# Kernel tuning notes

Measured on AMD Instinct MI355X. Metric: run time of the kernel, lower is better.

## Reference

```python
import jax, jax.numpy as jnp
import numpy as np

N_EMBD = 1024
N_HEAD = 16
HEAD = N_EMBD // N_HEAD


def setup_inputs() -> dict:
    key = jax.random.key(0)
    ks = jax.random.split(key, 5)
    B, T = 2, 2048
    s = 1.0 / np.sqrt(N_EMBD)
    return {
        "x": jax.random.normal(ks[0], (B, T, N_EMBD), dtype=jnp.float32),
        "w_attn": jax.random.normal(ks[1], (N_EMBD, 3 * N_EMBD), dtype=jnp.float32) * s,
        "b_attn": jnp.zeros((3 * N_EMBD,), dtype=jnp.float32),
        "w_proj": jax.random.normal(ks[2], (N_EMBD, N_EMBD), dtype=jnp.float32) * s,
        "b_proj": jnp.zeros((N_EMBD,), dtype=jnp.float32),
    }


def reference(x, w_attn, b_attn, w_proj, b_proj):
    B, T, C = x.shape
    qkv = x @ w_attn + b_attn                      # [B,T,3C]
    q, k, v = jnp.split(qkv, 3, axis=-1)
    def heads(t):
        return t.reshape(B, T, N_HEAD, HEAD).transpose(0, 2, 1, 3)  # [B,H,T,D]
    q, k, v = heads(q), heads(k), heads(v)
    scale = 1.0 / np.sqrt(HEAD).astype(np.float32)
    scores = jnp.einsum('bhqd,bhkd->bhqk', q, k) * scale
    causal = jnp.tril(jnp.ones((T, T), dtype=bool))
    scores = jnp.where(causal, scores, -jnp.inf)
    attn = jax.nn.softmax(scores, axis=-1)
    out = jnp.einsum('bhqk,bhkd->bhqd', attn, v)   # [B,H,T,D]
    out = out.transpose(0, 2, 1, 3).reshape(B, T, C)
    return out @ w_proj + b_proj
```

## Files before the change

### kernel.cpp

```cpp
#include <hip/hip_runtime.h>
#include <stdint.h>

#define N_EMBD 1024
#define N_HEADv 16
#define HEADv 64
#define Bv 2
#define Tv 2048
#define BT (Bv*Tv)
#define C3 (3*N_EMBD)

typedef __attribute__((ext_vector_type(8))) short bf16x8;
typedef __attribute__((ext_vector_type(4))) float f32x4;

typedef __attribute__((address_space(3))) uint32_t lds_u32;
typedef const __attribute__((address_space(1))) uint32_t glb_u32;

__device__ __forceinline__ void gload_lds16(const void* g, void* l){
  __builtin_amdgcn_global_load_lds((glb_u32*)g, (lds_u32*)l, 16, 0, 0);
}

__device__ __forceinline__ unsigned short f2bf(float f){
  union { float f; uint32_t u; } v; v.f = f;
  uint32_t u = v.u;
  uint32_t r = u + 0x7FFFu + ((u>>16)&1u);
  return (unsigned short)(r>>16);
}
__device__ __forceinline__ uint32_t f2bf_fast(float f){
  union { float f; uint32_t u; } v; v.f = f;
  return (v.u + 0x8000u) >> 16;
}
__device__ __forceinline__ float bf2f(unsigned short s){
  union { uint32_t u; float f; } v; v.u = ((uint32_t)s)<<16; return v.f;
}

__global__ void k_cvt_bf16(const float* __restrict__ in, unsigned short* __restrict__ out, long n){
  long i = ((long)blockIdx.x*blockDim.x + threadIdx.x)*8;
  if(i >= n) return;
  float4 a = *reinterpret_cast<const float4*>(in+i);
  float4 b = *reinterpret_cast<const float4*>(in+i+4);
  union { int4 v; unsigned short s[8]; } o;
  o.s[0]=f2bf(a.x); o.s[1]=f2bf(a.y); o.s[2]=f2bf(a.z); o.s[3]=f2bf(a.w);
  o.s[4]=f2bf(b.x); o.s[5]=f2bf(b.y); o.s[6]=f2bf(b.z); o.s[7]=f2bf(b.w);
  *reinterpret_cast<int4*>(out+i) = o.v;
}

__global__ void k_transpose_bf16(const float* __restrict__ in, unsigned short* __restrict__ out, int K, int N){
  __shared__ float tile[64][65];
  int n0 = blockIdx.x*64, k0 = blockIdx.y*64;
  int t = threadIdx.x;
  #pragma unroll
  for(int p=0;p<4;p++){
    int row = (t>>4) + p*16;
    int col4 = (t&15)*4;
    float4 v = *reinterpret_cast<const float4*>(&in[(size_t)(k0+row)*N + n0 + col4]);
    tile[row][col4+0]=v.x; tile[row][col4+1]=v.y; tile[row][col4+2]=v.z; tile[row][col4+3]=v.w;
  }
  __syncthreads();
  #pragma unroll
  for(int p=0;p<4;p++){
    int nrow = (t>>4) + p*16;
    int kc = (t&15)*4;
    ushort4 o;
    o.x = f2bf(tile[kc+0][nrow]);
    o.y = f2bf(tile[kc+1][nrow]);
    o.z = f2bf(tile[kc+2][nrow]);
    o.w = f2bf(tile[kc+3][nrow]);
    *reinterpret_cast<ushort4*>(&out[(size_t)(n0+nrow)*K + k0 + kc]) = o;
  }
}

template<int MODE>
__global__ __launch_bounds__(256) void k_gemm(
    const unsigned short* __restrict__ A,
    const unsigned short* __restrict__ Bt,
    const float* __restrict__ bias,
    void* __restrict__ Cout,
    int M, int N, int K)
{
  const int BK=64;
  const int TSZ=128*BK;
  __shared__ unsigned short As[2*TSZ];
  __shared__ unsigned short Bs[2*TSZ];
  int m0 = blockIdx.y*128, n0 = blockIdx.x*128;
  int t = threadIdx.x, lane = t&63, wid = t>>6;
  int wm = (wid>>1)*64, wn = (wid&1)*64;
  int g = lane>>4, r16 = lane&15;
  int rl  = lane>>3;
  int cle = (((lane&7) ^ rl) * 8);
  int rsw = r16 & 7;
  f32x4 acc[4][4] = {};

  #pragma unroll
  for(int c=0;c<4;c++){
    int rb = wid*32 + c*8;
    gload_lds16(&A [(size_t)(m0+rb+rl)*K + cle], &As[rb*BK]);
    gload_lds16(&Bt[(size_t)(n0+rb+rl)*K + cle], &Bs[rb*BK]);
  }
  __syncthreads();

  const int NIT = K/BK;
  for(int it=0; it<NIT; ++it){
    int cur = it & 1;
    if(it+1 < NIT){
      int k0 = (it+1)*BK;
      int nxt = (cur^1)*TSZ;
      #pragma unroll
      for(int c=0;c<4;c++){
        int rb = wid*32 + c*8;
        gload_lds16(&A [(size_t)(m0+rb+rl)*K + k0 + cle], &As[nxt + rb*BK]);
        gload_lds16(&Bt[(size_t)(n0+rb+rl)*K + k0 + cle], &Bs[nxt + rb*BK]);
      }
    }
    const unsigned short* Ab = &As[cur*TSZ];
    const unsigned short* Bb = &Bs[cur*TSZ];
    bf16x8 af[2][4], bfr[2][4];
    #pragma unroll
    for(int ks=0;ks<2;ks++){
      #pragma unroll
      for(int mi=0;mi<4;mi++)
        af[ks][mi]  = *reinterpret_cast<const bf16x8*>(&Ab[(wm+mi*16+r16)*BK + (((ks*4+g)^rsw)*8)]);
      #pragma unroll
      for(int ni=0;ni<4;ni++)
        bfr[ks][ni] = *reinterpret_cast<const bf16x8*>(&Bb[(wn+ni*16+r16)*BK + (((ks*4+g)^rsw)*8)]);
    }
    __builtin_amdgcn_s_setprio(1);
    #pragma unroll
    for(int ks=0;ks<2;ks++)
      #pragma unroll
      for(int mi=0;mi<4;mi++)
        #pragma unroll
        for(int ni=0;ni<4;ni++){
          if(MODE==0)
            acc[mi][ni] = __builtin_amdgcn_mfma_f32_16x16x32_bf16(af[ks][mi], bfr[ks][ni], acc[mi][ni], 0,0,0);
          else
            acc[mi][ni] = __builtin_amdgcn_mfma_f32_16x16x32_bf16(bfr[ks][ni], af[ks][mi], acc[mi][ni], 0,0,0);
        }
    __builtin_amdgcn_s_setprio(0);
    __syncthreads();
  }

  if(MODE==0){
    int which = (n0+wn)>>10;
    int h = ((n0+wn)&1023)>>6;
    int bb = m0>>11;
    int tt0 = (m0&2047) + wm;
    unsigned short* base = (unsigned short*)Cout;
    if(which < 2){
      unsigned short* dst = base + (size_t)which*BT*N_EMBD
                          + (((size_t)bb*N_HEADv + h)*Tv + tt0)*HEADv;
      #pragma unroll
      for(int ni=0;ni<4;ni++){
        float bv = bias[n0+wn+ni*16+r16];
        int d = ni*16 + r16;
        #pragma unroll
        for(int mi=0;mi<4;mi++)
          #pragma unroll
          for(int reg=0;reg<4;reg++){
            int tt = mi*16 + g*4 + reg;
            dst[(size_t)tt*HEADv + d] = f2bf(acc[mi][ni][reg] + bv);
          }
      }
    } else {
      unsigned short* dst = base + 2ll*BT*N_EMBD
                          + (((size_t)bb*N_HEADv + h)*HEADv)*Tv + tt0;
      #pragma unroll
      for(int ni=0;ni<4;ni++){
        float bv = bias[n0+wn+ni*16+r16];
        int d = ni*16 + r16;
        #pragma unroll
        for(int mi=0;mi<4;mi++)
          #pragma unroll
          for(int reg=0;reg<4;reg++){
            int tt = mi*16 + g*4 + reg;
            dst[(size_t)d*Tv + tt] = f2bf(acc[mi][ni][reg] + bv);
          }
      }
    }
  } else {
    float* out = (float*)Cout;
    #pragma unroll
    for(int mi=0;mi<4;mi++){
      int m = m0+wm+mi*16+r16;
      #pragma unroll
      for(int ni=0;ni<4;ni++){
        int n = n0+wn+ni*16+g*4;
        float4 b4 = *reinterpret_cast<const float4*>(&bias[n]);
        float4 o4;
        o4.x = acc[mi][ni][0] + b4.x;
        o4.y = acc[mi][ni][1] + b4.y;
        o4.z = acc[mi][ni][2] + b4.z;
        o4.w = acc[mi][ni][3] + b4.w;
        *reinterpret_cast<float4*>(&out[(size_t)m*N + n]) = o4;
      }
    }
  }
}

__global__ __launch_bounds__(256) void k_attn(
    const unsigned short* __restrict__ QKV,
    unsigned short* __restrict__ O,
    unsigned short* __restrict__ partO,
    float2* __restrict__ stats)
{
  __shared__ unsigned short Ks[2][64][64];
  __shared__ unsigned short Vs[2][64][64];
  __shared__ unsigned short Ps[4][16][64];
  int blk = blockIdx.x;
  int bh = blk & 31;
  int j  = blk >> 5;
  int qt, kt0, ktN; bool single;
  if(j < 16)      { qt = 16+j;  kt0 = 0;  ktN = 16;    single = false; }
  else if(j < 32) { qt = 47-j;  kt0 = 16; ktN = qt+1;  single = false; }
  else            { qt = 47-j;  kt0 = 0;  ktN = qt+1;  single = true;  }

  int t = threadIdx.x, lane=t&63, wid=t>>6;
  int g = lane>>4, r16 = lane&15;
  const unsigned short* Qp  = QKV + (size_t)bh*Tv*HEADv;
  const unsigned short* Kp  = QKV + (size_t)BT*N_EMBD + (size_t)bh*Tv*HEADv;
  const unsigned short* Vtp = QKV + 2ll*BT*N_EMBD + (size_t)bh*HEADv*Tv;
  int q0 = qt*64 + wid*16;

  bf16x8 aq[2];
  #pragma unroll
  for(int kb=0;kb<2;kb++)
    aq[kb] = *reinterpret_cast<const bf16x8*>(&Qp[(size_t)(q0+r16)*HEADv + kb*32 + g*8]);

  f32x4 oacc[4] = {};
  float m2 = -1e30f, l = 0.f;

  int r0 = t>>3, c0 = (t&7)*8;
  int r1 = r0 + 32;
  int sw0 = c0 ^ ((r0&7)<<3);
  int sw1 = c0 ^ ((r1&7)<<3);
  int rsw = (r16&7)<<3;

  int4 kc0, kc1, vc0, vc1;
  kc0 = *reinterpret_cast<const int4*>(&Kp [(size_t)(kt0*64+r0)*HEADv + c0]);
  kc1 = *reinterpret_cast<const int4*>(&Kp [(size_t)(kt0*64+r1)*HEADv + c0]);
  vc0 = *reinterpret_cast<const int4*>(&Vtp[(size_t)r0*Tv + kt0*64 + c0]);
  vc1 = *reinterpret_cast<const int4*>(&Vtp[(size_t)r1*Tv + kt0*64 + c0]);
  *reinterpret_cast<int4*>(&Ks[0][r0][sw0]) = kc0;
  *reinterpret_cast<int4*>(&Ks[0][r1][sw1]) = kc1;
  *reinterpret_cast<int4*>(&Vs[0][r0][sw0]) = vc0;
  *reinterpret_cast<int4*>(&Vs[0][r1][sw1]) = vc1;
  if(ktN - kt0 > 1){
    kc0 = *reinterpret_cast<const int4*>(&Kp [(size_t)((kt0+1)*64+r0)*HEADv + c0]);
    kc1 = *reinterpret_cast<const int4*>(&Kp [(size_t)((kt0+1)*64+r1)*HEADv + c0]);
    vc0 = *reinterpret_cast<const int4*>(&Vtp[(size_t)r0*Tv + (kt0+1)*64 + c0]);
    vc1 = *reinterpret_cast<const int4*>(&Vtp[(size_t)r1*Tv + (kt0+1)*64 + c0]);
  }
  __syncthreads();

  for(int kt=kt0; kt<ktN; ++kt){
    int cur = kt & 1;
    if(kt+1 < ktN){
      *reinterpret_cast<int4*>(&Ks[cur^1][r0][sw0]) = kc0;
      *reinterpret_cast<int4*>(&Ks[cur^1][r1][sw1]) = kc1;
      *reinterpret_cast<int4*>(&Vs[cur^1][r0][sw0]) = vc0;
      *reinterpret_cast<int4*>(&Vs[cur^1][r1][sw1]) = vc1;
      if(kt+2 < ktN){
        kc0 = *reinterpret_cast<const int4*>(&Kp [(size_t)((kt+2)*64+r0)*HEADv + c0]);
        kc1 = *reinterpret_cast<const int4*>(&Kp [(size_t)((kt+2)*64+r1)*HEADv + c0]);
        vc0 = *reinterpret_cast<const int4*>(&Vtp[(size_t)r0*Tv + (kt+2)*64 + c0]);
        vc1 = *reinterpret_cast<const int4*>(&Vtp[(size_t)r1*Tv + (kt+2)*64 + c0]);
      }
    }

    f32x4 sacc[4];
    __builtin_amdgcn_s_setprio(1);
    #pragma unroll
    for(int nb=0;nb<4;nb++){
      sacc[nb] = (f32x4){0.f,0.f,0.f,0.f};
      #pragma unroll
      for(int kb=0;kb<2;kb++){
        bf16x8 bk = *reinterpret_cast<const bf16x8*>(&Ks[cur][nb*16+r16][(kb*32+g*8) ^ rsw]);
        sacc[nb] = __builtin_amdgcn_mfma_f32_16x16x32_bf16(bk, aq[kb], sacc[nb],0,0,0);
      }
    }
    __builtin_amdgcn_s_setprio(0);

    const float SC = 0.18033688f;
    bool diag = (kt == qt);
    float pv[4][4];
    float mxnb[4];
    #pragma unroll
    for(int nb=0;nb<4;nb++){
      #pragma unroll
      for(int reg=0;reg<4;reg++){
        float s = sacc[nb][reg] * SC;
        if(diag){
          int keyin = nb*16 + g*4 + reg;
          if(keyin > wid*16 + r16) s = -1e30f;
        }
        pv[nb][reg] = s;
      }
      mxnb[nb] = fmaxf(fmaxf(pv[nb][0],pv[nb][1]), fmaxf(pv[nb][2],pv[nb][3]));
    }
    float mx = fmaxf(fmaxf(mxnb[0],mxnb[1]), fmaxf(mxnb[2],mxnb[3]));
    mx = fmaxf(mx, __shfl_xor(mx, 16, 64));
    mx = fmaxf(mx, __shfl_xor(mx, 32, 64));

    if(!__all(mx - m2 <= 11.5f)){
      float mn = fmaxf(m2, mx);
      float alpha = __builtin_amdgcn_exp2f(m2 - mn);
      l *= alpha;
      #pragma unroll
      for(int nb=0;nb<4;nb++)
        #pragma unroll
        for(int reg=0;reg<4;reg++) oacc[nb][reg] *= alpha;
      m2 = mn;
    }

    float rsnb[4];
    #pragma unroll
    for(int nb=0;nb<4;nb++){
      #pragma unroll
      for(int reg=0;reg<4;reg++)
        pv[nb][reg] = __builtin_amdgcn_exp2f(pv[nb][reg] - m2);
      rsnb[nb] = (pv[nb][0]+pv[nb][1]) + (pv[nb][2]+pv[nb][3]);
    }
    float rs = (rsnb[0]+rsnb[1]) + (rsnb[2]+rsnb[3]);
    rs += __shfl_xor(rs, 16, 64);
    rs += __shfl_xor(rs, 32, 64);
    l += rs;

    #pragma unroll
    for(int nb=0;nb<4;nb++){
      union { uint32_t u[2]; int2 v; } w;
      w.u[0] = f2bf_fast(pv[nb][0]) | (f2bf_fast(pv[nb][1])<<16);
      w.u[1] = f2bf_fast(pv[nb][2]) | (f2bf_fast(pv[nb][3])<<16);
      *reinterpret_cast<int2*>(&Ps[wid][r16][(nb*16+g*4) ^ rsw]) = w.v;
    }

    __builtin_amdgcn_s_setprio(1);
    #pragma unroll
    for(int kb=0;kb<2;kb++){
      bf16x8 ap = *reinterpret_cast<const bf16x8*>(&Ps[wid][r16][(kb*32+g*8) ^ rsw]);
      #pragma unroll
      for(int nb=0;nb<4;nb++){
        bf16x8 bv = *reinterpret_cast<const bf16x8*>(&Vs[cur][nb*16+r16][(kb*32+g*8) ^ rsw]);
        oacc[nb] = __builtin_amdgcn_mfma_f32_16x16x32_bf16(bv, ap, oacc[nb],0,0,0);
      }
    }
    __builtin_amdgcn_s_setprio(0);
    __syncthreads();
  }

  float rinv = 1.0f / l;
  if(single){
    int b = bh >> 4, h = bh & 15;
    size_t row = (size_t)b*Tv + q0 + r16;
    #pragma unroll
    for(int nb=0;nb<4;nb++){
      ushort4 o;
      o.x = f2bf(oacc[nb][0]*rinv);
      o.y = f2bf(oacc[nb][1]*rinv);
      o.z = f2bf(oacc[nb][2]*rinv);
      o.w = f2bf(oacc[nb][3]*rinv);
      *reinterpret_cast<ushort4*>(&O[row*N_EMBD + h*HEADv + nb*16 + g*4]) = o;
    }
  } else {
    int part = j*32 + bh;
    unsigned short* po = partO + (size_t)part*4096;
    int qloc = wid*16 + r16;
    #pragma unroll
    for(int nb=0;nb<4;nb++){
      ushort4 o;
      o.x = f2bf(oacc[nb][0]*rinv);
      o.y = f2bf(oacc[nb][1]*rinv);
      o.z = f2bf(oacc[nb][2]*rinv);
      o.w = f2bf(oacc[nb][3]*rinv);
      *reinterpret_cast<ushort4*>(&po[qloc*64 + nb*16 + g*4]) = o;
    }
    if(g==0) stats[part*64 + qloc] = make_float2(m2, l);
  }
}

__global__ __launch_bounds__(256) void k_merge(
    const unsigned short* __restrict__ partO,
    const float2* __restrict__ stats,
    unsigned short* __restrict__ O)
{
  int blk = blockIdx.x;
  int bh = blk & 31, qt = 16 + (blk >> 5);
  int p0 = (qt-16)*32 + bh;
  int p1 = (47-qt)*32 + bh;
  int t = threadIdx.x;
  int q = t >> 2, d0 = (t&3)*16;
  float2 s0 = stats[p0*64 + q];
  float2 s1 = stats[p1*64 + q];
  float m = fmaxf(s0.x, s1.x);
  float w0 = s0.y * __builtin_amdgcn_exp2f(s0.x - m);
  float w1 = s1.y * __builtin_amdgcn_exp2f(s1.x - m);
  float rinv = 1.f/(w0+w1);
  w0 *= rinv; w1 *= rinv;
  const unsigned short* a = partO + (size_t)p0*4096 + q*64 + d0;
  const unsigned short* b = partO + (size_t)p1*4096 + q*64 + d0;
  int bb = bh >> 4, h = bh & 15;
  unsigned short* o = O + ((size_t)bb*Tv + qt*64 + q)*N_EMBD + h*HEADv + d0;
  #pragma unroll
  for(int half=0; half<2; ++half){
    union { int4 v; unsigned short s[8]; } ua, ub, uo;
    ua.v = *reinterpret_cast<const int4*>(a + half*8);
    ub.v = *reinterpret_cast<const int4*>(b + half*8);
    #pragma unroll
    for(int e=0;e<8;e++)
      uo.s[e] = f2bf(bf2f(ua.s[e])*w0 + bf2f(ub.s[e])*w1);
    *reinterpret_cast<int4*>(o + half*8) = uo.v;
  }
}

extern "C" void kernel_launch(void* const* d_in, const int* in_sizes, int n_in,
                              void* d_out, int out_size, void* d_ws, size_t ws_size,
                              hipStream_t stream){
  const float* x      = (const float*)d_in[0];
  const float* w_attn = (const float*)d_in[1];
  const float* b_attn = (const float*)d_in[2];
  const float* w_proj = (const float*)d_in[3];
  const float* b_proj = (const float*)d_in[4];
  char* ws = (char*)d_ws;
  unsigned short* xb  = (unsigned short*)ws;
  unsigned short* qkv = (unsigned short*)(ws + 8ll*1024*1024);
  unsigned short* ob  = (unsigned short*)(ws + 32ll*1024*1024);
  unsigned short* wat = (unsigned short*)(ws + 40ll*1024*1024);
  unsigned short* wpt = (unsigned short*)(ws + 46ll*1024*1024);
  unsigned short* partO = xb;
  float2*        stats  = (float2*)wat;

  k_cvt_bf16<<<2048,256,0,stream>>>(x, xb, (long)BT*N_EMBD);
  k_transpose_bf16<<<dim3(C3/64, N_EMBD/64),256,0,stream>>>(w_attn, wat, N_EMBD, C3);
  k_transpose_bf16<<<dim3(N_EMBD/64, N_EMBD/64),256,0,stream>>>(w_proj, wpt, N_EMBD, N_EMBD);
  k_gemm<0><<<dim3(C3/128, BT/128),256,0,stream>>>(xb, wat, b_attn, (void*)qkv, BT, C3, N_EMBD);
  k_attn<<<dim3(48*32),256,0,stream>>>(qkv, ob, partO, stats);
  k_merge<<<dim3(512),256,0,stream>>>(partO, stats, ob);
  k_gemm<1><<<dim3(N_EMBD/128, BT/128),256,0,stream>>>(ob, wpt, b_proj, d_out, BT, N_EMBD, N_EMBD);
}
```

Baseline: 123.0 us.

## Fold softmax scale into Q, speculate exp with fixed max, row-sum via MFMA

The softmax scale (including log2e) is folded into Q in the QKV GEMM epilogue, which removes a multiply per score. Exponentials are now computed speculatively against the running max (initialised to a fixed 6.0) before the max reduction, and are recomputed only when the max jumps past the threshold. The row-sum reduction with shuffles is replaced by an extra MFMA that multiplies a ones vector by the P tile. This removes ALU and shuffle work from the critical path, at the cost of an occasional exp recompute and some dependence on score magnitudes staying near the fixed initial max.

Result: no change. 121.4 us (-1.3%).

```diff
diff --git a/kernel.cpp b/kernel.cpp
--- a/kernel.cpp
+++ b/kernel.cpp
@@ -146,6 +146,7 @@
     int tt0 = (m0&2047) + wm;
     unsigned short* base = (unsigned short*)Cout;
     if(which < 2){
+      float scale = (which==0) ? 0.18033688f : 1.0f;
       unsigned short* dst = base + (size_t)which*BT*N_EMBD
                           + (((size_t)bb*N_HEADv + h)*Tv + tt0)*HEADv;
       #pragma unroll
@@ -157,7 +158,7 @@
           #pragma unroll
           for(int reg=0;reg<4;reg++){
             int tt = mi*16 + g*4 + reg;
-            dst[(size_t)tt*HEADv + d] = f2bf(acc[mi][ni][reg] + bv);
+            dst[(size_t)tt*HEADv + d] = f2bf((acc[mi][ni][reg] + bv)*scale);
           }
       }
     } else {
@@ -225,8 +226,12 @@
   for(int kb=0;kb<2;kb++)
     aq[kb] = *reinterpret_cast<const bf16x8*>(&Qp[(size_t)(q0+r16)*HEADv + kb*32 + g*8]);
 
+  const short ONE = (short)0x3F80;
+  const bf16x8 ones8 = {ONE,ONE,ONE,ONE,ONE,ONE,ONE,ONE};
+
   f32x4 oacc[4] = {};
-  float m2 = -1e30f, l = 0.f;
+  f32x4 lacc = {};
+  float m2 = 6.0f;
 
   int r0 = t>>3, c0 = (t&7)*8;
   int r1 = r0 + 32;
@@ -279,23 +284,29 @@
     }
     __builtin_amdgcn_s_setprio(0);
 
-    const float SC = 0.18033688f;
     bool diag = (kt == qt);
-    float pv[4][4];
-    float mxnb[4];
-    #pragma unroll
-    for(int nb=0;nb<4;nb++){
+    float sv[4][4], pv[4][4];
+    #pragma unroll
+    for(int nb=0;nb<4;nb++)
       #pragma unroll
       for(int reg=0;reg<4;reg++){
-        float s = sacc[nb][reg] * SC;
+        float s = sacc[nb][reg];
         if(diag){
           int keyin = nb*16 + g*4 + reg;
           if(keyin > wid*16 + r16) s = -1e30f;
         }
-        pv[nb][reg] = s;
-      }
-      mxnb[nb] = fmaxf(fmaxf(pv[nb][0],pv[nb][1]), fmaxf(pv[nb][2],pv[nb][3]));
-    }
+        sv[nb][reg] = s;
+      }
+    #pragma unroll
+    for(int nb=0;nb<4;nb++)
+      #pragma unroll
+      for(int reg=0;reg<4;reg++)
+        pv[nb][reg] = __builtin_amdgcn_exp2f(sv[nb][reg] - m2);
+
+    float mxnb[4];
+    #pragma unroll
+    for(int nb=0;nb<4;nb++)
+      mxnb[nb] = fmaxf(fmaxf(sv[nb][0],sv[nb][1]), fmaxf(sv[nb][2],sv[nb][3]));
     float mx = fmaxf(fmaxf(mxnb[0],mxnb[1]), fmaxf(mxnb[2],mxnb[3]));
     mx = fmaxf(mx, __shfl_xor(mx, 16, 64));
     mx = fmaxf(mx, __shfl_xor(mx, 32, 64));
@@ -303,26 +314,18 @@
     if(!__all(mx - m2 <= 11.5f)){
       float mn = fmaxf(m2, mx);
       float alpha = __builtin_amdgcn_exp2f(m2 - mn);
-      l *= alpha;
+      lacc[0]*=alpha; lacc[1]*=alpha; lacc[2]*=alpha; lacc[3]*=alpha;
       #pragma unroll
       for(int nb=0;nb<4;nb++)
         #pragma unroll
         for(int reg=0;reg<4;reg++) oacc[nb][reg] *= alpha;
       m2 = mn;
-    }
-
-    float rsnb[4];
-    #pragma unroll
-    for(int nb=0;nb<4;nb++){
-      #pragma unroll
-      for(int reg=0;reg<4;reg++)
-        pv[nb][reg] = __builtin_amdgcn_exp2f(pv[nb][reg] - m2);
-      rsnb[nb] = (pv[nb][0]+pv[nb][1]) + (pv[nb][2]+pv[nb][3]);
-    }
-    float rs = (rsnb[0]+rsnb[1]) + (rsnb[2]+rsnb[3]);
-    rs += __shfl_xor(rs, 16, 64);
-    rs += __shfl_xor(rs, 32, 64);
-    l += rs;
+      #pragma unroll
+      for(int nb=0;nb<4;nb++)
+        #pragma unroll
+        for(int reg=0;reg<4;reg++)
+          pv[nb][reg] = __builtin_amdgcn_exp2f(sv[nb][reg] - m2);
+    }
 
     #pragma unroll
     for(int nb=0;nb<4;nb++){
@@ -336,6 +339,7 @@
     #pragma unroll
     for(int kb=0;kb<2;kb++){
       bf16x8 ap = *reinterpret_cast<const bf16x8*>(&Ps[wid][r16][(kb*32+g*8) ^ rsw]);
+      lacc = __builtin_amdgcn_mfma_f32_16x16x32_bf16(ones8, ap, lacc,0,0,0);
       #pragma unroll
       for(int nb=0;nb<4;nb++){
         bf16x8 bv = *reinterpret_cast<const bf16x8*>(&Vs[cur][nb*16+r16][(kb*32+g*8) ^ rsw]);
@@ -346,6 +350,7 @@
     __syncthreads();
   }
 
+  float l = lacc[0];
   float rinv = 1.0f / l;
   if(single){
     int b = bh >> 4, h = bh & 15;
```
